# Kernel optimization log

Measured on AMD Instinct MI355X. Metric: run time of the kernel, lower is better.

## Reference

```python
import jax, jax.numpy as jnp
import numpy as np

NB_CLUSTERS = 128   # C: number of clusters (equal-size, sorted ids)
PTS_PER_CLUSTER = 1024  # P: points per cluster
DIM = 3


def setup_inputs() -> dict:
    key = jax.random.key(0)
    k1, k2 = jax.random.split(key)
    n = NB_CLUSTERS * PTS_PER_CLUSTER
    input_points = jax.random.normal(k1, (n, DIM), dtype=jnp.float32)
    output_points = jax.random.normal(k2, (n, DIM), dtype=jnp.float32)
    clusters = jnp.repeat(jnp.arange(NB_CLUSTERS, dtype=jnp.int32), PTS_PER_CLUSTER)
    return {
        "input_points": input_points,
        "input_clusters": clusters,
        "output_points": output_points,
        "output_clusters": clusters,
    }


def reference(input_points, input_clusters, output_points, output_clusters):
    # Original: nb_clusters = max(input_clusters); loop for i in range(nb_clusters)
    # -> the HIGHEST cluster id is excluded from the loss. Reproduced via mask.
    nb = jnp.max(input_clusters)  # == NB_CLUSTERS - 1
    a = input_points.reshape(NB_CLUSTERS, PTS_PER_CLUSTER, DIM)   # [C,P,3]
    b = output_points.reshape(NB_CLUSTERS, PTS_PER_CLUSTER, DIM)  # [C,P,3]

    # Pairwise squared distances per cluster: d[c,i,j] = ||a[c,i]-b[c,j]||^2
    d = (jnp.sum(a * a, axis=-1)[:, :, None]
         + jnp.sum(b * b, axis=-1)[:, None, :]
         - 2.0 * jnp.einsum('cid,cjd->cij', a, b))  # [C,P,P]

    # Indices computed under no_grad in the original (ints: no grad anyway).
    idx1 = jnp.argmin(d, axis=2)  # for each input point: nearest output point
    idx2 = jnp.argmin(d, axis=1)  # for each output point: nearest input point

    near_b = jnp.take_along_axis(b, idx1[..., None], axis=1)  # [C,P,3]
    near_a = jnp.take_along_axis(a, idx2[..., None], axis=1)  # [C,P,3]

    l1 = jnp.sum((a - near_b) ** 2, axis=(1, 2))  # [C]
    l2 = jnp.sum((b - near_a) ** 2, axis=(1, 2))  # [C]

    mask = (jnp.arange(NB_CLUSTERS) < nb).astype(a.dtype)  # exclude last cluster
    return jnp.sum(mask * (l1 + l2))
```

## Files before the change

kernel.cpp:

```cpp
#include <hip/hip_runtime.h>


#define PTS 1024
#define ACTIVE_CLUSTERS 127
#define QG   64
#define Q    16
#define SEG  16
#define TPB  1024
#define TSEG (PTS / SEG)

__global__ __launch_bounds__(TPB) void chamfer_kernel(
    const float* __restrict__ pts_in,
    const float* __restrict__ pts_out,
    float* __restrict__ out)
{
    const int c   = blockIdx.x >> 1;
    const int dir = blockIdx.x & 1;

    const float* __restrict__ query  = dir ? pts_out : pts_in;
    const float* __restrict__ target = dir ? pts_in  : pts_out;

    __shared__ __align__(16) float4 st[PTS];
    __shared__ float pm[SEG * Q * QG];

    const int tid = threadIdx.x;
    const int qi  = tid & (QG - 1);
    const int seg = tid >> 6;
    const size_t base = (size_t)c * PTS * 3;

    {
        const float* tp = target + base + (size_t)tid * 3;
        float x = tp[0], y = tp[1], z = tp[2];
        st[tid] = make_float4(x, y, z, fmaf(x, x, fmaf(y, y, z * z)));
    }

    float qx[Q], qy[Q], qz[Q], qn[Q], mn[Q];
    #pragma unroll
    for (int k = 0; k < Q; ++k) {
        const float* qp = query + base + (size_t)(k * QG + qi) * 3;
        float ax = qp[0], ay = qp[1], az = qp[2];
        qn[k] = fmaf(ax, ax, fmaf(ay, ay, az * az));
        qx[k] = -2.0f * ax;
        qy[k] = -2.0f * ay;
        qz[k] = -2.0f * az;
        mn[k] = 3.4e38f;
    }
    __syncthreads();

    const int j0 = seg * TSEG;
    #pragma unroll 2
    for (int jj = 0; jj < TSEG; jj += 2) {
        const float4 b0 = st[j0 + jj];
        const float4 b1 = st[j0 + jj + 1];
        #pragma unroll
        for (int k = 0; k < Q; ++k) {
            float s0 = fmaf(qx[k], b0.x, b0.w);
            s0 = fmaf(qy[k], b0.y, s0);
            s0 = fmaf(qz[k], b0.z, s0);
            float s1 = fmaf(qx[k], b1.x, b1.w);
            s1 = fmaf(qy[k], b1.y, s1);
            s1 = fmaf(qz[k], b1.z, s1);
            mn[k] = fminf(fminf(s0, s1), mn[k]);
        }
    }

    #pragma unroll
    for (int k = 0; k < Q; ++k)
        pm[(seg * Q + k) * QG + qi] = mn[k] + qn[k];
    __syncthreads();

    const int k2  = tid >> 6;
    const int qi2 = tid & (QG - 1);
    float v = 3.4e38f;
    #pragma unroll
    for (int s = 0; s < SEG; ++s)
        v = fminf(v, pm[(s * Q + k2) * QG + qi2]);

    #pragma unroll
    for (int off = 32; off > 0; off >>= 1)
        v += __shfl_down(v, off, 64);

    __shared__ float wsum[16];
    const int wave = tid >> 6;
    const int lane = tid & 63;
    if (lane == 0) wsum[wave] = v;
    __syncthreads();

    if (wave == 0) {
        float t = (lane < 16) ? wsum[lane] : 0.0f;
        #pragma unroll
        for (int off = 8; off > 0; off >>= 1)
            t += __shfl_down(t, off, 64);
        if (lane == 0) atomicAdd(out, t);
    }
}

extern "C" void kernel_launch(void* const* d_in, const int* in_sizes, int n_in,
                              void* d_out, int out_size, void* d_ws, size_t ws_size,
                              hipStream_t stream) {
    const float* input_points  = (const float*)d_in[0];
    const float* output_points = (const float*)d_in[2];
    float* out = (float*)d_out;

    hipMemsetAsync(out, 0, sizeof(float), stream);

    chamfer_kernel<<<dim3(ACTIVE_CLUSTERS * 2), dim3(TPB), 0, stream>>>(
        input_points, output_points, out);
}
```

Measured before the change: 83.47 us.

## Split each cluster-direction into four query blocks for more parallelism

Each cluster/direction pair is now split across four blocks of 512 threads, each handling 256 query points with 8 queries per thread instead of 16. Grid size grows from 254 to 1016 blocks so work spreads across more CUs, and register pressure per thread drops so more waves can be resident. The query norms are no longer held in registers; they are recomputed at the end from a fresh global load. The cost is that each block reloads the full target cluster into shared memory, so target loading and the atomic adds both grow fourfold.

```diff
diff --git a/kernel.cpp b/kernel.cpp
--- a/kernel.cpp
+++ b/kernel.cpp
@@ -3,19 +3,23 @@
 
 #define PTS 1024
 #define ACTIVE_CLUSTERS 127
-#define QG   64
-#define Q    16
+#define QG   32
+#define Q    8
 #define SEG  16
-#define TPB  1024
+#define TPB  512
 #define TSEG (PTS / SEG)
+#define QB   (Q * QG)
+#define NQB  (PTS / QB)
 
-__global__ __launch_bounds__(TPB) void chamfer_kernel(
+__global__ __launch_bounds__(TPB, 8) void chamfer_kernel(
     const float* __restrict__ pts_in,
     const float* __restrict__ pts_out,
     float* __restrict__ out)
 {
-    const int c   = blockIdx.x >> 1;
-    const int dir = blockIdx.x & 1;
+    const int b   = blockIdx.x;
+    const int c   = b >> 3;
+    const int dir = (b >> 2) & 1;
+    const int qb  = b & 3;
 
     const float* __restrict__ query  = dir ? pts_out : pts_in;
     const float* __restrict__ target = dir ? pts_in  : pts_out;
@@ -25,30 +29,27 @@
 
     const int tid = threadIdx.x;
     const int qi  = tid & (QG - 1);
-    const int seg = tid >> 6;
+    const int seg = tid >> 5;
     const size_t base = (size_t)c * PTS * 3;
 
-    {
-        const float* tp = target + base + (size_t)tid * 3;
+    for (int t = tid; t < PTS; t += TPB) {
+        const float* tp = target + base + (size_t)t * 3;
         float x = tp[0], y = tp[1], z = tp[2];
-        st[tid] = make_float4(x, y, z, fmaf(x, x, fmaf(y, y, z * z)));
+        st[t] = make_float4(x, y, z, fmaf(x, x, fmaf(y, y, z * z)));
     }
 
-    float qx[Q], qy[Q], qz[Q], qn[Q], mn[Q];
+    float qx[Q], qy[Q], qz[Q], mn[Q];
     #pragma unroll
     for (int k = 0; k < Q; ++k) {
-        const float* qp = query + base + (size_t)(k * QG + qi) * 3;
-        float ax = qp[0], ay = qp[1], az = qp[2];
-        qn[k] = fmaf(ax, ax, fmaf(ay, ay, az * az));
-        qx[k] = -2.0f * ax;
-        qy[k] = -2.0f * ay;
-        qz[k] = -2.0f * az;
+        const float* qp = query + base + (size_t)(qb * QB + k * QG + qi) * 3;
+        qx[k] = -2.0f * qp[0];
+        qy[k] = -2.0f * qp[1];
+        qz[k] = -2.0f * qp[2];
         mn[k] = 3.4e38f;
     }
     __syncthreads();
 
     const int j0 = seg * TSEG;
-    #pragma unroll 2
     for (int jj = 0; jj < TSEG; jj += 2) {
         const float4 b0 = st[j0 + jj];
         const float4 b1 = st[j0 + jj + 1];
@@ -66,30 +67,36 @@
 
     #pragma unroll
     for (int k = 0; k < Q; ++k)
-        pm[(seg * Q + k) * QG + qi] = mn[k] + qn[k];
+        pm[(seg * Q + k) * QG + qi] = mn[k];
     __syncthreads();
 
-    const int k2  = tid >> 6;
-    const int qi2 = tid & (QG - 1);
-    float v = 3.4e38f;
-    #pragma unroll
-    for (int s = 0; s < SEG; ++s)
-        v = fminf(v, pm[(s * Q + k2) * QG + qi2]);
+    float v = 0.0f;
+    if (tid < QB) {
+        const int k2  = tid >> 5;
+        const int qi2 = tid & (QG - 1);
+        float m = 3.4e38f;
+        #pragma unroll
+        for (int s = 0; s < SEG; ++s)
+            m = fminf(m, pm[(s * Q + k2) * QG + qi2]);
+        const float* qp = query + base + (size_t)(qb * QB + tid) * 3;
+        float ax = qp[0], ay = qp[1], az = qp[2];
+        v = m + fmaf(ax, ax, fmaf(ay, ay, az * az));
+    }
 
     #pragma unroll
     for (int off = 32; off > 0; off >>= 1)
         v += __shfl_down(v, off, 64);
 
-    __shared__ float wsum[16];
+    __shared__ float wsum[8];
     const int wave = tid >> 6;
     const int lane = tid & 63;
     if (lane == 0) wsum[wave] = v;
     __syncthreads();
 
     if (wave == 0) {
-        float t = (lane < 16) ? wsum[lane] : 0.0f;
+        float t = (lane < 8) ? wsum[lane] : 0.0f;
         #pragma unroll
-        for (int off = 8; off > 0; off >>= 1)
+        for (int off = 4; off > 0; off >>= 1)
             t += __shfl_down(t, off, 64);
         if (lane == 0) atomicAdd(out, t);
     }
@@ -104,6 +111,6 @@
 
     hipMemsetAsync(out, 0, sizeof(float), stream);
 
-    chamfer_kernel<<<dim3(ACTIVE_CLUSTERS * 2), dim3(TPB), 0, stream>>>(
+    chamfer_kernel<<<dim3(ACTIVE_CLUSTERS * 2 * NQB), dim3(TPB), 0, stream>>>(
         input_points, output_points, out);
 }
```

Result: no change. 83.96 us (+0.6%).
